# Kernel tuning notes

Hardware: AMD Instinct MI355X
Metric: run time of the kernel (lower is better)

## Reference

```python
import jax, jax.numpy as jnp
import numpy as np

N = 100000   # nodes per type
E = 400000   # edges per relation
D = 128      # in_dim == out_dim
H = 4        # heads
DK = D // H  # 32
EPS = 1e-5


def setup_inputs() -> dict:
    key = jax.random.key(0)
    ks = jax.random.split(key, 16)
    s = 1.0 / np.sqrt(D)  # fan-in scaling for stable activations
    inp = {
        "x_drug": jax.random.normal(ks[0], (N, D), jnp.float32),
        "x_dis": jax.random.normal(ks[1], (N, D), jnp.float32),
        "Wp_drug": jax.random.normal(ks[2], (D, D), jnp.float32) * s,
        "bp_drug": jnp.zeros((D,), jnp.float32),
        "Wp_dis": jax.random.normal(ks[3], (D, D), jnp.float32) * s,
        "bp_dis": jnp.zeros((D,), jnp.float32),
        "Wk_r0": jax.random.normal(ks[4], (D, D), jnp.float32) * s,
        "Wv_r0": jax.random.normal(ks[5], (D, D), jnp.float32) * s,
        "Wk_r1": jax.random.normal(ks[6], (D, D), jnp.float32) * s,
        "Wv_r1": jax.random.normal(ks[7], (D, D), jnp.float32) * s,
        "Wu_drug": jax.random.normal(ks[8], (D, D), jnp.float32) * s,
        "bu_drug": jnp.zeros((D,), jnp.float32),
        "Wu_dis": jax.random.normal(ks[9], (D, D), jnp.float32) * s,
        "bu_dis": jnp.zeros((D,), jnp.float32),
        "g_drug": jnp.ones((D,), jnp.float32),
        "be_drug": jnp.zeros((D,), jnp.float32),
        "g_dis": jnp.ones((D,), jnp.float32),
        "be_dis": jnp.zeros((D,), jnp.float32),
        "ei_r0": jax.random.randint(ks[10], (2, E), 0, N, jnp.int32),  # drug -> dis
        "ei_r1": jax.random.randint(ks[11], (2, E), 0, N, jnp.int32),  # dis  -> drug
    }
    return inp


def _rel_attention(h_src_all, h_dst_all, ei, Wk, Wv, n_dst):
    # gather -> per-relation K/V proj -> edge softmax over dst -> scatter-add
    src, dst = ei[0], ei[1]
    h_src = h_src_all[src]                                  # [E, D]
    Q = h_dst_all[dst].reshape(-1, H, DK)                   # [E, H, DK]
    K = (h_src @ Wk).reshape(-1, H, DK)
    V = (h_src @ Wv).reshape(-1, H, DK)
    scores = jnp.sum(Q * K, axis=-1) / np.sqrt(DK)          # [E, H]
    # scatter_softmax over destination groups (numerically stable)
    m = jax.lax.stop_gradient(
        jax.ops.segment_max(scores, dst, num_segments=n_dst))  # [N, H]
    ex = jnp.exp(scores - m[dst])
    ssum = jax.ops.segment_sum(ex, dst, num_segments=n_dst)    # [N, H]
    attn = ex / ssum[dst]                                      # [E, H]
    wV = (V * attn[..., None]).reshape(-1, D)                  # [E, D]
    return jax.ops.segment_sum(wV, dst, num_segments=n_dst)    # [N, D]


def _update(h, agg, Wu, bu, g, be):
    x = h + (agg @ Wu + bu)  # skip + update (dropout=0)
    mu = jnp.mean(x, axis=-1, keepdims=True)
    var = jnp.var(x, axis=-1, keepdims=True)
    ln = (x - mu) * jax.lax.rsqrt(var + EPS) * g + be
    return jax.nn.relu(ln)


def reference(x_drug, x_dis, Wp_drug, bp_drug, Wp_dis, bp_dis,
              Wk_r0, Wv_r0, Wk_r1, Wv_r1,
              Wu_drug, bu_drug, Wu_dis, bu_dis,
              g_drug, be_drug, g_dis, be_dis, ei_r0, ei_r1):
    # type-specific projection
    h_drug = x_drug @ Wp_drug + bp_drug
    h_dis = x_dis @ Wp_dis + bp_dis
    # per-relation attention + intra/inter-type aggregation
    agg_dis = _rel_attention(h_drug, h_dis, ei_r0, Wk_r0, Wv_r0, N)
    agg_drug = _rel_attention(h_dis, h_drug, ei_r1, Wk_r1, Wv_r1, N)
    out_drug = _update(h_drug, agg_drug, Wu_drug, bu_drug, g_drug, be_drug)
    out_dis = _update(h_dis, agg_dis, Wu_dis, bu_dis, g_dis, be_dis)
    return jnp.stack([out_drug, out_dis])  # [2, N, D]
```

## Files before the change

kernel.cpp:

```cpp
#include <hip/hip_runtime.h>
#include <math.h>

#define NN 100000
#define EE 400000
#define DD 128

typedef __attribute__((ext_vector_type(8))) short bf16x8;
typedef __attribute__((ext_vector_type(4))) float f32x4;

#if defined(__has_builtin)
#if __has_builtin(__builtin_amdgcn_fdot2_f32_bf16)
#define HAVE_FDOT2 1
typedef __attribute__((ext_vector_type(2))) __bf16 bf16x2t;
#endif
#endif

__device__ __forceinline__ unsigned short f2bf(float f) {
  unsigned u = __float_as_uint(f);
  u += 0x7FFF + ((u >> 16) & 1);
  return (unsigned short)(u >> 16);
}
__device__ __forceinline__ float bf2f(unsigned short u) {
  return __uint_as_float(((unsigned)u) << 16);
}

__global__ __launch_bounds__(256) void prep_weights(
    const float* __restrict__ Wp_dr, const float* __restrict__ bp_dr,
    const float* __restrict__ Wp_di, const float* __restrict__ bp_di,
    const float* __restrict__ Wu_dr, const float* __restrict__ Wu_di,
    const float* __restrict__ Bk0, const float* __restrict__ Bv0,
    const float* __restrict__ Bk1, const float* __restrict__ Bv1,
    unsigned short* __restrict__ Wpt_dr, unsigned short* __restrict__ Wpt_di,
    unsigned short* __restrict__ Wut_dr, unsigned short* __restrict__ Wut_di,
    unsigned short* __restrict__ Wkt0, float* __restrict__ bk0,
    unsigned short* __restrict__ Wvt0, float* __restrict__ bv0,
    unsigned short* __restrict__ Wkt1, float* __restrict__ bk1,
    unsigned short* __restrict__ Wvt1, float* __restrict__ bv1) {
  const int b = blockIdx.x, t = threadIdx.x;
  if (b < 256) {
    const int id = b * 256 + t;
    const int m = id >> 14, rem = id & 16383, k = rem & 127, c = rem >> 7;
    const float* W = (m == 0) ? Wp_dr : (m == 1) ? Wp_di : (m == 2) ? Wu_dr : Wu_di;
    unsigned short* O = (m == 0) ? Wpt_dr : (m == 1) ? Wpt_di : (m == 2) ? Wut_dr : Wut_di;
    O[c * DD + k] = f2bf(W[(size_t)k * DD + c]);
  } else if (b < 512) {
    const int id = (b - 256) * 256 + t;
    const int m = id >> 14, rem = id & 16383, k = rem & 127, c = rem >> 7;
    const float* A = (m < 2) ? Wp_dr : Wp_di;
    const float* B = (m == 0) ? Bk0 : (m == 1) ? Bv0 : (m == 2) ? Bk1 : Bv1;
    unsigned short* O = (m == 0) ? Wkt0 : (m == 1) ? Wvt0 : (m == 2) ? Wkt1 : Wvt1;
    const float4* a4 = (const float4*)(A + (size_t)k * DD);
    float s = 0.0f;
#pragma unroll 8
    for (int j4 = 0; j4 < 32; ++j4) {
      const float4 av = a4[j4];
      s += av.x * B[(4 * j4 + 0) * DD + c] + av.y * B[(4 * j4 + 1) * DD + c]
         + av.z * B[(4 * j4 + 2) * DD + c] + av.w * B[(4 * j4 + 3) * DD + c];
    }
    O[c * DD + k] = f2bf(s);
  } else {
    const int id = (b - 512) * 256 + t;
    if (id < 512) {
      const int m = id >> 7, c = id & 127;
      const float* bp = (m < 2) ? bp_dr : bp_di;
      const float* B = (m == 0) ? Bk0 : (m == 1) ? Bv0 : (m == 2) ? Bk1 : Bv1;
      float* bo = (m == 0) ? bk0 : (m == 1) ? bv0 : (m == 2) ? bk1 : bv1;
      float s = 0.0f;
#pragma unroll 8
      for (int j = 0; j < DD; ++j) s += bp[j] * B[j * DD + c];
      bo[c] = s;
    }
  }
}

#define STAGE_W(SRC)                                                          \
  do {                                                                        \
    __syncthreads();                                                          \
    _Pragma("unroll") for (int i_ = threadIdx.x; i_ < 2048; i_ += 256) {      \
      const int L_ = i_ * 16;                                                 \
      *(float4*)((char*)WL + (L_ ^ (((L_ >> 8) & 7) << 4))) =                 \
          ((const float4*)(SRC))[i_];                                         \
    }                                                                         \
    __syncthreads();                                                          \
  } while (0)

__device__ __forceinline__ void mfma_tile_store(
    const unsigned short* WL, const bf16x8* a, int lane, int rowbase,
    bool wvalid, const float* __restrict__ bias,
    unsigned short* __restrict__ outb) {
  const int r0 = rowbase + (lane >> 4) * 4;
#pragma unroll
  for (int ni = 0; ni < 8; ++ni) {
    const int cl = ni * 16 + (lane & 15);
    f32x4 acc = {0.f, 0.f, 0.f, 0.f};
#pragma unroll
    for (int kk = 0; kk < 4; ++kk) {
      int boff = cl * 256 + kk * 64 + (lane >> 4) * 16;
      boff ^= (cl & 7) << 4;
      const bf16x8 bb = *(const bf16x8*)((const char*)WL + boff);
      acc = __builtin_amdgcn_mfma_f32_16x16x32_bf16(a[kk], bb, acc, 0, 0, 0);
    }
    if (wvalid) {
      const float bv = bias[cl];
#pragma unroll
      for (int r = 0; r < 4; ++r)
        outb[(size_t)(r0 + r) * DD + cl] = f2bf(acc[r] + bv);
    }
  }
}

__global__ __launch_bounds__(256) void fused_proj(
    const float* __restrict__ x0, const unsigned short* __restrict__ Wpt0,
    const float* __restrict__ bp0, const unsigned short* __restrict__ Wkta,
    const float* __restrict__ bka, const unsigned short* __restrict__ Wvta,
    const float* __restrict__ bva, unsigned short* __restrict__ h0,
    unsigned short* __restrict__ K0, unsigned short* __restrict__ V0,
    const float* __restrict__ x1, const unsigned short* __restrict__ Wpt1,
    const float* __restrict__ bp1, const unsigned short* __restrict__ Wktb,
    const float* __restrict__ bkb, const unsigned short* __restrict__ Wvtb,
    const float* __restrict__ bvb, unsigned short* __restrict__ h1,
    unsigned short* __restrict__ K1, unsigned short* __restrict__ V1, int half) {
  __shared__ unsigned short WL[DD * DD];
  int bid = blockIdx.x;
  const bool second = bid >= half;
  if (second) bid -= half;
  const float* x = second ? x1 : x0;
  const unsigned short* Wpt = second ? Wpt1 : Wpt0;
  const float* bpv = second ? bp1 : bp0;
  const unsigned short* Wkt = second ? Wktb : Wkta;
  const float* bkv = second ? bkb : bka;
  const unsigned short* Wvt = second ? Wvtb : Wvta;
  const float* bvv = second ? bvb : bva;
  unsigned short* h = second ? h1 : h0;
  unsigned short* K = second ? K1 : K0;
  unsigned short* V = second ? V1 : V0;

  const int tid = threadIdx.x, lane = tid & 63, wid = tid >> 6;
  const int rowbase = bid * 64 + wid * 16;
  const bool wvalid = rowbase < NN;
  bf16x8 a[4];
  if (wvalid) {
    const int arow = rowbase + (lane & 15);
    const float* xr = x + (size_t)arow * DD + (lane >> 4) * 8;
#pragma unroll
    for (int kk = 0; kk < 4; ++kk) {
      const float4 f0 = *(const float4*)(xr + kk * 32);
      const float4 f1 = *(const float4*)(xr + kk * 32 + 4);
      a[kk][0] = (short)f2bf(f0.x); a[kk][1] = (short)f2bf(f0.y);
      a[kk][2] = (short)f2bf(f0.z); a[kk][3] = (short)f2bf(f0.w);
      a[kk][4] = (short)f2bf(f1.x); a[kk][5] = (short)f2bf(f1.y);
      a[kk][6] = (short)f2bf(f1.z); a[kk][7] = (short)f2bf(f1.w);
    }
  } else {
#pragma unroll
    for (int kk = 0; kk < 4; ++kk)
#pragma unroll
      for (int j = 0; j < 8; ++j) a[kk][j] = 0;
  }
  STAGE_W(Wpt);
  mfma_tile_store(WL, a, lane, rowbase, wvalid, bpv, h);
  STAGE_W(Wkt);
  mfma_tile_store(WL, a, lane, rowbase, wvalid, bkv, K);
  STAGE_W(Wvt);
  mfma_tile_store(WL, a, lane, rowbase, wvalid, bvv, V);
}

__global__ __launch_bounds__(256) void update_ln2(
    const unsigned short* __restrict__ hA, const unsigned short* __restrict__ aggA,
    const unsigned short* __restrict__ WutA, const float* __restrict__ buA,
    const float* __restrict__ gA, const float* __restrict__ beA,
    float* __restrict__ outA,
    const unsigned short* __restrict__ hB, const unsigned short* __restrict__ aggB,
    const unsigned short* __restrict__ WutB, const float* __restrict__ buB,
    const float* __restrict__ gB, const float* __restrict__ beB,
    float* __restrict__ outB, int half) {
  __shared__ unsigned short WL[DD * DD];
  int bid = blockIdx.x;
  const bool second = bid >= half;
  if (second) bid -= half;
  const unsigned short* h = second ? hB : hA;
  const unsigned short* agg = second ? aggB : aggA;
  const unsigned short* Wut = second ? WutB : WutA;
  const float* bu = second ? buB : buA;
  const float* g = second ? gB : gA;
  const float* be = second ? beB : beA;
  float* out = second ? outB : outA;

  const int tid = threadIdx.x, lane = tid & 63, wid = tid >> 6;
  const int rowbase = bid * 64 + wid * 16;
  const bool wvalid = rowbase < NN;
  bf16x8 a[4];
  if (wvalid) {
    const int arow = rowbase + (lane & 15);
#pragma unroll
    for (int kk = 0; kk < 4; ++kk)
      a[kk] = *(const bf16x8*)(agg + (size_t)arow * DD + kk * 32 + (lane >> 4) * 8);
  } else {
#pragma unroll
    for (int kk = 0; kk < 4; ++kk)
#pragma unroll
      for (int j = 0; j < 8; ++j) a[kk][j] = 0;
  }
  STAGE_W(Wut);
  f32x4 acc[8];
  const int r0 = rowbase + (lane >> 4) * 4;
#pragma unroll
  for (int ni = 0; ni < 8; ++ni) {
    const int cl = ni * 16 + (lane & 15);
    acc[ni] = (f32x4){0.f, 0.f, 0.f, 0.f};
#pragma unroll
    for (int kk = 0; kk < 4; ++kk) {
      int boff = cl * 256 + kk * 64 + (lane >> 4) * 16;
      boff ^= (cl & 7) << 4;
      const bf16x8 bb = *(const bf16x8*)((const char*)WL + boff);
      acc[ni] = __builtin_amdgcn_mfma_f32_16x16x32_bf16(a[kk], bb, acc[ni], 0, 0, 0);
    }
  }
  if (!wvalid) return;
#pragma unroll
  for (int ni = 0; ni < 8; ++ni) {
    const int cl = ni * 16 + (lane & 15);
    const float bv = bu[cl];
#pragma unroll
    for (int r = 0; r < 4; ++r)
      acc[ni][r] += bf2f(h[(size_t)(r0 + r) * DD + cl]) + bv;
  }
  float mean[4], inv[4];
#pragma unroll
  for (int r = 0; r < 4; ++r) {
    float s = 0.f, q = 0.f;
#pragma unroll
    for (int ni = 0; ni < 8; ++ni) {
      const float v = acc[ni][r];
      s += v; q += v * v;
    }
    s += __shfl_xor(s, 1); q += __shfl_xor(q, 1);
    s += __shfl_xor(s, 2); q += __shfl_xor(q, 2);
    s += __shfl_xor(s, 4); q += __shfl_xor(q, 4);
    s += __shfl_xor(s, 8); q += __shfl_xor(q, 8);
    const float mu = s * (1.0f / 128.0f);
    mean[r] = mu;
    inv[r] = rsqrtf(q * (1.0f / 128.0f) - mu * mu + 1e-5f);
  }
#pragma unroll
  for (int ni = 0; ni < 8; ++ni) {
    const int cl = ni * 16 + (lane & 15);
    const float gv = g[cl], bev = be[cl];
#pragma unroll
    for (int r = 0; r < 4; ++r)
      out[(size_t)(r0 + r) * DD + cl] =
          fmaxf((acc[ni][r] - mean[r]) * inv[r] * gv + bev, 0.0f);
  }
}

__global__ __launch_bounds__(256) void count_deg2(const int* __restrict__ ei0,
                                                  const int* __restrict__ ei1,
                                                  int* __restrict__ deg) {
  const int e = blockIdx.x * 256 + threadIdx.x;
  if (e >= 2 * EE) return;
  const int d = (e < EE) ? ei0[EE + e] : (NN + ei1[e]);
  atomicAdd(&deg[d], 1);
}

__global__ __launch_bounds__(256) void scan1(const int* __restrict__ deg,
                                             int* __restrict__ excl,
                                             int* __restrict__ partials, int n) {
  __shared__ int ls[256];
  const int b0 = blockIdx.x * 1024;
  const int t = threadIdx.x;
  int v[4];
  int s = 0;
#pragma unroll
  for (int i = 0; i < 4; ++i) {
    const int idx = b0 + t * 4 + i;
    v[i] = (idx < n) ? deg[idx] : 0;
    s += v[i];
  }
  ls[t] = s;
  __syncthreads();
  for (int off = 1; off < 256; off <<= 1) {
    const int x = (t >= off) ? ls[t - off] : 0;
    __syncthreads();
    ls[t] += x;
    __syncthreads();
  }
  int ex = ls[t] - s;
#pragma unroll
  for (int i = 0; i < 4; ++i) {
    const int idx = b0 + t * 4 + i;
    if (idx < n) excl[idx] = ex;
    ex += v[i];
  }
  if (t == 255) partials[blockIdx.x] = ls[255];
}

__global__ __launch_bounds__(256) void scan2(int* __restrict__ partials, int nb) {
  __shared__ int ls[256];
  const int t = threadIdx.x;
  const int v = (t < nb) ? partials[t] : 0;
  ls[t] = v;
  __syncthreads();
  for (int off = 1; off < 256; off <<= 1) {
    const int x = (t >= off) ? ls[t - off] : 0;
    __syncthreads();
    ls[t] += x;
    __syncthreads();
  }
  if (t < nb) partials[t] = ls[t] - v;
}

__global__ __launch_bounds__(256) void scan3(const int* __restrict__ excl,
                                             const int* __restrict__ partials,
                                             int n, int* __restrict__ rowptr,
                                             int* __restrict__ cursor) {
  const int i = blockIdx.x * 256 + threadIdx.x;
  if (i < n) {
    const int v = excl[i] + partials[i >> 10];
    rowptr[i] = v;
    cursor[i] = v;
  }
  if (i == 0) rowptr[n] = 2 * EE;
}

__global__ __launch_bounds__(256) void fill_csr2(const int* __restrict__ ei0,
                                                 const int* __restrict__ ei1,
                                                 int* __restrict__ cursor,
                                                 int* __restrict__ csr_src) {
  const int e = blockIdx.x * 256 + threadIdx.x;
  if (e >= 2 * EE) return;
  int s, d;
  if (e < EE) { s = ei0[e]; d = ei0[EE + e]; }
  else        { s = ei1[e - EE]; d = NN + ei1[e]; }
  const int p = atomicAdd(&cursor[d], 1);
  csr_src[p] = s;
}

__global__ __launch_bounds__(256) void dst_attention(
    const unsigned short* __restrict__ Hq0, const unsigned short* __restrict__ K0,
    const unsigned short* __restrict__ V0, unsigned short* __restrict__ agg0,
    const unsigned short* __restrict__ Hq1, const unsigned short* __restrict__ K1,
    const unsigned short* __restrict__ V1, unsigned short* __restrict__ agg1,
    const int* __restrict__ rowptr, const int* __restrict__ csr_src) {
  const int gw = blockIdx.x * 4 + (threadIdx.x >> 6);
  if (gw >= 2 * NN) return;
  const bool rel1 = gw >= NN;
  const int node = rel1 ? gw - NN : gw;
  const unsigned short* Hq = rel1 ? Hq1 : Hq0;
  const unsigned short* K = rel1 ? K1 : K0;
  const unsigned short* V = rel1 ? V1 : V0;
  unsigned short* agg = rel1 ? agg1 : agg0;

  const int lane = threadIdx.x & 63;
  const int sub = lane & 15;
  const int grp = lane >> 4;
  const int beg = rowptr[gw], end = rowptr[gw + 1];
  const uint4 qu = *(const uint4*)(Hq + (size_t)node * DD + sub * 8);
#if defined(HAVE_FDOT2)
  const bf16x2t q0 = __builtin_bit_cast(bf16x2t, qu.x);
  const bf16x2t q1 = __builtin_bit_cast(bf16x2t, qu.y);
  const bf16x2t q2 = __builtin_bit_cast(bf16x2t, qu.z);
  const bf16x2t q3 = __builtin_bit_cast(bf16x2t, qu.w);
#else
  float qf[8];
  qf[0] = bf2f((unsigned short)qu.x); qf[1] = bf2f((unsigned short)(qu.x >> 16));
  qf[2] = bf2f((unsigned short)qu.y); qf[3] = bf2f((unsigned short)(qu.y >> 16));
  qf[4] = bf2f((unsigned short)qu.z); qf[5] = bf2f((unsigned short)(qu.z >> 16));
  qf[6] = bf2f((unsigned short)qu.w); qf[7] = bf2f((unsigned short)(qu.w >> 16));
#endif
  float av[8] = {0.f, 0.f, 0.f, 0.f, 0.f, 0.f, 0.f, 0.f};
  float lsum = 0.0f;
  for (int i = beg + grp; i < end; i += 4) {
    const int sidx = csr_src[i];
    const uint4 kp = *(const uint4*)(K + (size_t)sidx * DD + sub * 8);
#if defined(HAVE_FDOT2)
    float p = __builtin_amdgcn_fdot2_f32_bf16(__builtin_bit_cast(bf16x2t, kp.x), q0, 0.0f, false);
    p = __builtin_amdgcn_fdot2_f32_bf16(__builtin_bit_cast(bf16x2t, kp.y), q1, p, false);
    p = __builtin_amdgcn_fdot2_f32_bf16(__builtin_bit_cast(bf16x2t, kp.z), q2, p, false);
    p = __builtin_amdgcn_fdot2_f32_bf16(__builtin_bit_cast(bf16x2t, kp.w), q3, p, false);
#else
    float p;
    p  = qf[0] * bf2f((unsigned short)kp.x) + qf[1] * bf2f((unsigned short)(kp.x >> 16));
    p += qf[2] * bf2f((unsigned short)kp.y) + qf[3] * bf2f((unsigned short)(kp.y >> 16));
    p += qf[4] * bf2f((unsigned short)kp.z) + qf[5] * bf2f((unsigned short)(kp.z >> 16));
    p += qf[6] * bf2f((unsigned short)kp.w) + qf[7] * bf2f((unsigned short)(kp.w >> 16));
#endif
    p += __shfl_xor(p, 1);
    p += __shfl_xor(p, 2);
    const float wgt = __expf(p * 0.17677669529663689f);
    const uint4 vp = *(const uint4*)(V + (size_t)sidx * DD + sub * 8);
    lsum += wgt;
    av[0] += wgt * __uint_as_float(vp.x << 16);
    av[1] += wgt * __uint_as_float(vp.x & 0xFFFF0000u);
    av[2] += wgt * __uint_as_float(vp.y << 16);
    av[3] += wgt * __uint_as_float(vp.y & 0xFFFF0000u);
    av[4] += wgt * __uint_as_float(vp.z << 16);
    av[5] += wgt * __uint_as_float(vp.z & 0xFFFF0000u);
    av[6] += wgt * __uint_as_float(vp.w << 16);
    av[7] += wgt * __uint_as_float(vp.w & 0xFFFF0000u);
  }
#pragma unroll
  for (int d = 0; d < 8; ++d) {
    av[d] += __shfl_xor(av[d], 16);
    av[d] += __shfl_xor(av[d], 32);
  }
  lsum += __shfl_xor(lsum, 16);
  lsum += __shfl_xor(lsum, 32);
  if (grp == 0) {
    const float invl = (lsum > 0.0f) ? (1.0f / lsum) : 0.0f;
    uint4 o;
    o.x = (unsigned)f2bf(av[0] * invl) | ((unsigned)f2bf(av[1] * invl) << 16);
    o.y = (unsigned)f2bf(av[2] * invl) | ((unsigned)f2bf(av[3] * invl) << 16);
    o.z = (unsigned)f2bf(av[4] * invl) | ((unsigned)f2bf(av[5] * invl) << 16);
    o.w = (unsigned)f2bf(av[6] * invl) | ((unsigned)f2bf(av[7] * invl) << 16);
    *(uint4*)(agg + (size_t)node * DD + sub * 8) = o;
  }
}

extern "C" void kernel_launch(void* const* d_in, const int* in_sizes, int n_in,
                              void* d_out, int out_size, void* d_ws, size_t ws_size,
                              hipStream_t stream) {
  const float* x_drug  = (const float*)d_in[0];
  const float* x_dis   = (const float*)d_in[1];
  const float* Wp_drug = (const float*)d_in[2];
  const float* bp_drug = (const float*)d_in[3];
  const float* Wp_dis  = (const float*)d_in[4];
  const float* bp_dis  = (const float*)d_in[5];
  const float* Wk_r0   = (const float*)d_in[6];
  const float* Wv_r0   = (const float*)d_in[7];
  const float* Wk_r1   = (const float*)d_in[8];
  const float* Wv_r1   = (const float*)d_in[9];
  const float* Wu_drug = (const float*)d_in[10];
  const float* bu_drug = (const float*)d_in[11];
  const float* Wu_dis  = (const float*)d_in[12];
  const float* bu_dis  = (const float*)d_in[13];
  const float* g_drug  = (const float*)d_in[14];
  const float* be_drug = (const float*)d_in[15];
  const float* g_dis   = (const float*)d_in[16];
  const float* be_dis  = (const float*)d_in[17];
  const int* ei_r0     = (const int*)d_in[18];
  const int* ei_r1     = (const int*)d_in[19];

  float* out = (float*)d_out;
  float* out_drug = out;
  float* out_dis  = out + (size_t)NN * DD;

  const size_t ND = (size_t)NN * DD;
  char* w = (char*)d_ws;
  unsigned short* Kr0  = (unsigned short*)w; w += ND * 2;
  unsigned short* Vr0  = (unsigned short*)w; w += ND * 2;
  unsigned short* Kr1  = (unsigned short*)w; w += ND * 2;
  unsigned short* Vr1  = (unsigned short*)w; w += ND * 2;
  unsigned short* agdr = (unsigned short*)w; w += ND * 2;
  unsigned short* agdi = (unsigned short*)w; w += ND * 2;
  unsigned short* hb_dr = (unsigned short*)w; w += ND * 2;
  unsigned short* hb_di = (unsigned short*)w; w += ND * 2;
  unsigned short* Wpt_dr = (unsigned short*)w; w += DD * DD * 2;
  unsigned short* Wpt_di = (unsigned short*)w; w += DD * DD * 2;
  unsigned short* Wut_dr = (unsigned short*)w; w += DD * DD * 2;
  unsigned short* Wut_di = (unsigned short*)w; w += DD * DD * 2;
  unsigned short* Wkt0 = (unsigned short*)w; w += DD * DD * 2;
  unsigned short* Wvt0 = (unsigned short*)w; w += DD * DD * 2;
  unsigned short* Wkt1 = (unsigned short*)w; w += DD * DD * 2;
  unsigned short* Wvt1 = (unsigned short*)w; w += DD * DD * 2;
  float* bk0 = (float*)w; w += DD * 4;
  float* bv0 = (float*)w; w += DD * 4;
  float* bk1 = (float*)w; w += DD * 4;
  float* bv1 = (float*)w; w += DD * 4;
  int* deg      = (int*)w; w += 2 * NN * 4;
  int* excl     = (int*)w; w += 2 * NN * 4;
  int* rowptr   = (int*)w; w += (2 * NN + 1) * 4;
  int* cursor   = (int*)w; w += 2 * NN * 4;
  int* partials = (int*)w; w += 256 * 4;
  int* csr_src  = (int*)w; w += 2 * EE * 4;

  const int gemm_blocks = (NN + 63) / 64;
  const int edge_blocks2 = (2 * EE + 255) / 256;
  const int nchunks = (2 * NN + 1023) / 1024;
  const int n256 = (2 * NN + 255) / 256;
  const int attn_blocks = (2 * NN + 3) / 4;
  dim3 b256(256);

  prep_weights<<<514, b256, 0, stream>>>(
      Wp_drug, bp_drug, Wp_dis, bp_dis, Wu_drug, Wu_dis,
      Wk_r0, Wv_r0, Wk_r1, Wv_r1,
      Wpt_dr, Wpt_di, Wut_dr, Wut_di,
      Wkt0, bk0, Wvt0, bv0, Wkt1, bk1, Wvt1, bv1);

  fused_proj<<<2 * gemm_blocks, b256, 0, stream>>>(
      x_drug, Wpt_dr, bp_drug, Wkt0, bk0, Wvt0, bv0, hb_dr, Kr0, Vr0,
      x_dis,  Wpt_di, bp_dis,  Wkt1, bk1, Wvt1, bv1, hb_di, Kr1, Vr1,
      gemm_blocks);

  hipMemsetAsync(deg, 0, 2 * NN * sizeof(int), stream);
  count_deg2<<<edge_blocks2, b256, 0, stream>>>(ei_r0, ei_r1, deg);
  scan1<<<nchunks, b256, 0, stream>>>(deg, excl, partials, 2 * NN);
  scan2<<<1, b256, 0, stream>>>(partials, nchunks);
  scan3<<<n256, b256, 0, stream>>>(excl, partials, 2 * NN, rowptr, cursor);
  fill_csr2<<<edge_blocks2, b256, 0, stream>>>(ei_r0, ei_r1, cursor, csr_src);

  dst_attention<<<attn_blocks, b256, 0, stream>>>(
      hb_di, Kr0, Vr0, agdi,
      hb_dr, Kr1, Vr1, agdr,
      rowptr, csr_src);

  update_ln2<<<2 * gemm_blocks, b256, 0, stream>>>(
      hb_dr, agdr, Wut_dr, bu_drug, g_drug, be_drug, out_drug,
      hb_di, agdi, Wut_di, bu_dis,  g_dis,  be_dis,  out_dis,
      gemm_blocks);
}
```

Measured before the change: 300.0 us.

## Fold degree zeroing and counting into existing kernels, drop cursor array

Moves the degree memset into extra blocks of prep_weights and the degree-count atomics into leading blocks of fused_proj, removing a memset and a kernel launch. The separate cursor array is removed: fill_csr advances rowptr in place, and attention recovers the row start as end minus degree. The LDS swizzle is widened from 8 to 16 rows to cut bank conflicts, and a redundant leading barrier in update_ln2 is dropped. This couples independent stages and relies on correct stream ordering, with little gain expected beyond launch overhead.

```diff
diff --git a/kernel.cpp b/kernel.cpp
--- a/kernel.cpp
+++ b/kernel.cpp
@@ -35,7 +35,8 @@
     unsigned short* __restrict__ Wkt0, float* __restrict__ bk0,
     unsigned short* __restrict__ Wvt0, float* __restrict__ bv0,
     unsigned short* __restrict__ Wkt1, float* __restrict__ bk1,
-    unsigned short* __restrict__ Wvt1, float* __restrict__ bv1) {
+    unsigned short* __restrict__ Wvt1, float* __restrict__ bv1,
+    int* __restrict__ deg) {
   const int b = blockIdx.x, t = threadIdx.x;
   if (b < 256) {
     const int id = b * 256 + t;
@@ -58,7 +59,7 @@
          + av.z * B[(4 * j4 + 2) * DD + c] + av.w * B[(4 * j4 + 3) * DD + c];
     }
     O[c * DD + k] = f2bf(s);
-  } else {
+  } else if (b < 514) {
     const int id = (b - 512) * 256 + t;
     if (id < 512) {
       const int m = id >> 7, c = id & 127;
@@ -70,6 +71,9 @@
       for (int j = 0; j < DD; ++j) s += bp[j] * B[j * DD + c];
       bo[c] = s;
     }
+  } else {
+    const int id = (b - 514) * 256 + t;
+    if (id < 2 * NN) deg[id] = 0;
   }
 }
 
@@ -78,7 +82,7 @@
     __syncthreads();                                                          \
     _Pragma("unroll") for (int i_ = threadIdx.x; i_ < 2048; i_ += 256) {      \
       const int L_ = i_ * 16;                                                 \
-      *(float4*)((char*)WL + (L_ ^ (((L_ >> 8) & 7) << 4))) =                 \
+      *(float4*)((char*)WL + (L_ ^ (((L_ >> 8) & 15) << 4))) =                \
           ((const float4*)(SRC))[i_];                                         \
     }                                                                         \
     __syncthreads();                                                          \
@@ -95,8 +99,7 @@
     f32x4 acc = {0.f, 0.f, 0.f, 0.f};
 #pragma unroll
     for (int kk = 0; kk < 4; ++kk) {
-      int boff = cl * 256 + kk * 64 + (lane >> 4) * 16;
-      boff ^= (cl & 7) << 4;
+      const int boff = cl * 256 + ((kk * 64 + (lane >> 4) * 16) ^ ((cl & 15) << 4));
       const bf16x8 bb = *(const bf16x8*)((const char*)WL + boff);
       acc = __builtin_amdgcn_mfma_f32_16x16x32_bf16(a[kk], bb, acc, 0, 0, 0);
     }
@@ -119,9 +122,21 @@
     const float* __restrict__ bp1, const unsigned short* __restrict__ Wktb,
     const float* __restrict__ bkb, const unsigned short* __restrict__ Wvtb,
     const float* __restrict__ bvb, unsigned short* __restrict__ h1,
-    unsigned short* __restrict__ K1, unsigned short* __restrict__ V1, int half) {
+    unsigned short* __restrict__ K1, unsigned short* __restrict__ V1,
+    int half, int cntblocks,
+    const int* __restrict__ ei0, const int* __restrict__ ei1,
+    int* __restrict__ deg) {
   __shared__ unsigned short WL[DD * DD];
   int bid = blockIdx.x;
+  if (bid < cntblocks) {
+    const int e = bid * 256 + threadIdx.x;
+    if (e < 2 * EE) {
+      const int d = (e < EE) ? ei0[EE + e] : (NN + ei1[e]);
+      atomicAdd(&deg[d], 1);
+    }
+    return;
+  }
+  bid -= cntblocks;
   const bool second = bid >= half;
   if (second) bid -= half;
   const float* x = second ? x1 : x0;
@@ -201,7 +216,13 @@
 #pragma unroll
       for (int j = 0; j < 8; ++j) a[kk][j] = 0;
   }
-  STAGE_W(Wut);
+#pragma unroll
+  for (int i_ = tid; i_ < 2048; i_ += 256) {
+    const int L_ = i_ * 16;
+    *(float4*)((char*)WL + (L_ ^ (((L_ >> 8) & 15) << 4))) =
+        ((const float4*)Wut)[i_];
+  }
+  __syncthreads();
   f32x4 acc[8];
   const int r0 = rowbase + (lane >> 4) * 4;
 #pragma unroll
@@ -210,8 +231,7 @@
     acc[ni] = (f32x4){0.f, 0.f, 0.f, 0.f};
 #pragma unroll
     for (int kk = 0; kk < 4; ++kk) {
-      int boff = cl * 256 + kk * 64 + (lane >> 4) * 16;
-      boff ^= (cl & 7) << 4;
+      const int boff = cl * 256 + ((kk * 64 + (lane >> 4) * 16) ^ ((cl & 15) << 4));
       const bf16x8 bb = *(const bf16x8*)((const char*)WL + boff);
       acc[ni] = __builtin_amdgcn_mfma_f32_16x16x32_bf16(a[kk], bb, acc[ni], 0, 0, 0);
     }
@@ -251,15 +271,6 @@
       out[(size_t)(r0 + r) * DD + cl] =
           fmaxf((acc[ni][r] - mean[r]) * inv[r] * gv + bev, 0.0f);
   }
-}
-
-__global__ __launch_bounds__(256) void count_deg2(const int* __restrict__ ei0,
-                                                  const int* __restrict__ ei1,
-                                                  int* __restrict__ deg) {
-  const int e = blockIdx.x * 256 + threadIdx.x;
-  if (e >= 2 * EE) return;
-  const int d = (e < EE) ? ei0[EE + e] : (NN + ei1[e]);
-  atomicAdd(&deg[d], 1);
 }
 
 __global__ __launch_bounds__(256) void scan1(const int* __restrict__ deg,
@@ -311,27 +322,21 @@
 
 __global__ __launch_bounds__(256) void scan3(const int* __restrict__ excl,
                                              const int* __restrict__ partials,
-                                             int n, int* __restrict__ rowptr,
-                                             int* __restrict__ cursor) {
+                                             int n, int* __restrict__ rowptr) {
   const int i = blockIdx.x * 256 + threadIdx.x;
-  if (i < n) {
-    const int v = excl[i] + partials[i >> 10];
-    rowptr[i] = v;
-    cursor[i] = v;
-  }
-  if (i == 0) rowptr[n] = 2 * EE;
+  if (i < n) rowptr[i] = excl[i] + partials[i >> 10];
 }
 
 __global__ __launch_bounds__(256) void fill_csr2(const int* __restrict__ ei0,
                                                  const int* __restrict__ ei1,
-                                                 int* __restrict__ cursor,
+                                                 int* __restrict__ rowptr,
                                                  int* __restrict__ csr_src) {
   const int e = blockIdx.x * 256 + threadIdx.x;
   if (e >= 2 * EE) return;
   int s, d;
   if (e < EE) { s = ei0[e]; d = ei0[EE + e]; }
   else        { s = ei1[e - EE]; d = NN + ei1[e]; }
-  const int p = atomicAdd(&cursor[d], 1);
+  const int p = atomicAdd(&rowptr[d], 1);
   csr_src[p] = s;
 }
 
@@ -340,7 +345,8 @@
     const unsigned short* __restrict__ V0, unsigned short* __restrict__ agg0,
     const unsigned short* __restrict__ Hq1, const unsigned short* __restrict__ K1,
     const unsigned short* __restrict__ V1, unsigned short* __restrict__ agg1,
-    const int* __restrict__ rowptr, const int* __restrict__ csr_src) {
+    const int* __restrict__ rowptr, const int* __restrict__ deg,
+    const int* __restrict__ csr_src) {
   const int gw = blockIdx.x * 4 + (threadIdx.x >> 6);
   if (gw >= 2 * NN) return;
   const bool rel1 = gw >= NN;
@@ -353,7 +359,8 @@
   const int lane = threadIdx.x & 63;
   const int sub = lane & 15;
   const int grp = lane >> 4;
-  const int beg = rowptr[gw], end = rowptr[gw + 1];
+  const int end = rowptr[gw];
+  const int beg = end - deg[gw];
   const uint4 qu = *(const uint4*)(Hq + (size_t)node * DD + sub * 8);
 #if defined(HAVE_FDOT2)
   const bf16x2t q0 = __builtin_bit_cast(bf16x2t, qu.x);
@@ -469,39 +476,37 @@
   int* deg      = (int*)w; w += 2 * NN * 4;
   int* excl     = (int*)w; w += 2 * NN * 4;
   int* rowptr   = (int*)w; w += (2 * NN + 1) * 4;
-  int* cursor   = (int*)w; w += 2 * NN * 4;
   int* partials = (int*)w; w += 256 * 4;
   int* csr_src  = (int*)w; w += 2 * EE * 4;
 
   const int gemm_blocks = (NN + 63) / 64;
-  const int edge_blocks2 = (2 * EE + 255) / 256;
+  const int cnt_blocks = (2 * EE + 255) / 256;
   const int nchunks = (2 * NN + 1023) / 1024;
   const int n256 = (2 * NN + 255) / 256;
   const int attn_blocks = (2 * NN + 3) / 4;
+  const int zero_blocks = (2 * NN + 255) / 256;
   dim3 b256(256);
 
-  prep_weights<<<514, b256, 0, stream>>>(
+  prep_weights<<<514 + zero_blocks, b256, 0, stream>>>(
       Wp_drug, bp_drug, Wp_dis, bp_dis, Wu_drug, Wu_dis,
       Wk_r0, Wv_r0, Wk_r1, Wv_r1,
       Wpt_dr, Wpt_di, Wut_dr, Wut_di,
-      Wkt0, bk0, Wvt0, bv0, Wkt1, bk1, Wvt1, bv1);
-
-  fused_proj<<<2 * gemm_blocks, b256, 0, stream>>>(
+      Wkt0, bk0, Wvt0, bv0, Wkt1, bk1, Wvt1, bv1, deg);
+
+  fused_proj<<<cnt_blocks + 2 * gemm_blocks, b256, 0, stream>>>(
       x_drug, Wpt_dr, bp_drug, Wkt0, bk0, Wvt0, bv0, hb_dr, Kr0, Vr0,
       x_dis,  Wpt_di, bp_dis,  Wkt1, bk1, Wvt1, bv1, hb_di, Kr1, Vr1,
-      gemm_blocks);
-
-  hipMemsetAsync(deg, 0, 2 * NN * sizeof(int), stream);
-  count_deg2<<<edge_blocks2, b256, 0, stream>>>(ei_r0, ei_r1, deg);
+      gemm_blocks, cnt_blocks, ei_r0, ei_r1, deg);
+
   scan1<<<nchunks, b256, 0, stream>>>(deg, excl, partials, 2 * NN);
   scan2<<<1, b256, 0, stream>>>(partials, nchunks);
-  scan3<<<n256, b256, 0, stream>>>(excl, partials, 2 * NN, rowptr, cursor);
-  fill_csr2<<<edge_blocks2, b256, 0, stream>>>(ei_r0, ei_r1, cursor, csr_src);
+  scan3<<<n256, b256, 0, stream>>>(excl, partials, 2 * NN, rowptr);
+  fill_csr2<<<cnt_blocks, b256, 0, stream>>>(ei_r0, ei_r1, rowptr, csr_src);
 
   dst_attention<<<attn_blocks, b256, 0, stream>>>(
       hb_di, Kr0, Vr0, agdi,
       hb_dr, Kr1, Vr1, agdr,
-      rowptr, csr_src);
+      rowptr, deg, csr_src);
 
   update_ln2<<<2 * gemm_blocks, b256, 0, stream>>>(
       hb_dr, agdr, Wut_dr, bu_drug, g_drug, be_drug, out_drug,
```

After: 285.8 us. -4.8%, faster.
